# Optimization experiments

Hardware: AMD Instinct MI355X
Metric: run time of the kernel (lower is better)

The kernel has to match this reference:

```python
import jax, jax.numpy as jnp
import numpy as np

B, C, H, W = 8, 256, 64, 64
NH = 8
CM = 2048
EPS = 1e-5


def setup_inputs() -> dict:
    key = jax.random.key(0)
    ks = jax.random.split(key, 16)
    n = lambda k, s: (jax.random.normal(k, s, dtype=jnp.float32) * 0.02)
    return {
        'x': jax.random.normal(ks[0], (B, C, H, W), dtype=jnp.float32),
        'Wqkv': n(ks[1], (C, 3 * C)), 'bqkv': n(ks[2], (3 * C,)),
        'dw_w': n(ks[3], (C, 1, 3, 3)), 'dw_b': n(ks[4], (C,)),
        'Wproj': n(ks[5], (C, C)), 'bproj': n(ks[6], (C,)),
        'bn1_g': jnp.ones((C,), jnp.float32), 'bn1_b': jnp.zeros((C,), jnp.float32),
        'bn1_m': n(ks[7], (C,)), 'bn1_v': jax.random.uniform(ks[8], (C,), dtype=jnp.float32) + 0.5,
        'alpha1': jnp.ones((1,), jnp.float32),
        'Wfc1': n(ks[9], (C, CM)), 'bfc1': n(ks[10], (CM,)),
        'Wfc2': n(ks[11], (CM, C)), 'bfc2': n(ks[12], (C,)),
        'bn2_g': jnp.ones((C,), jnp.float32), 'bn2_b': jnp.zeros((C,), jnp.float32),
        'bn2_m': n(ks[13], (C,)), 'bn2_v': jax.random.uniform(ks[14], (C,), dtype=jnp.float32) + 0.5,
        'alpha2': jnp.ones((1,), jnp.float32),
    }


def _repbn(x, g, b, m, v, alpha):
    # eval-mode RepBN: BatchNorm1d with running stats over channel dim + alpha*x
    bn = (x - m) * jax.lax.rsqrt(v + EPS) * g + b
    return bn + alpha * x


def reference(x, Wqkv, bqkv, dw_w, dw_b, Wproj, bproj,
              bn1_g, bn1_b, bn1_m, bn1_v, alpha1,
              Wfc1, bfc1, Wfc2, bfc2,
              bn2_g, bn2_b, bn2_m, bn2_v, alpha2):
    b, c, h, w = x.shape
    n = h * w
    hd = c // NH
    scale = hd ** (-0.5)
    t = x.reshape(b, c, n).transpose(0, 2, 1)  # [B,N,C]

    # --- SimplifiedLinearAttention ---
    qkv = (t @ Wqkv + bqkv).reshape(b, n, 3, NH, hd).transpose(2, 0, 3, 1, 4)
    q, k, v = qkv[0], qkv[1], qkv[2]          # [B,H,N,hd]
    q = jax.nn.relu(q) * scale
    k = jax.nn.relu(k)
    ctx = jnp.einsum('bhnd,bhne->bhde', k, v)  # [B,H,hd,hd] small context
    out = jnp.einsum('bhnd,bhde->bhne', q, ctx)
    out = out.transpose(0, 2, 1, 3).reshape(b, n, c)
    img = out.transpose(0, 2, 1).reshape(b, c, h, w)
    img = jax.lax.conv_general_dilated(img, dw_w, (1, 1), 'SAME',
                                       feature_group_count=c)
    img = img + dw_b[None, :, None, None]
    out = img.reshape(b, c, n).transpose(0, 2, 1)
    out = out @ Wproj + bproj

    # residual + RepBN (eval branch of LinearNorm)
    t = _repbn(t + out, bn1_g, bn1_b, bn1_m, bn1_v, alpha1)

    # FFN (exact GELU as nn.GELU default)
    ff = jax.nn.gelu(t @ Wfc1 + bfc1, approximate=False) @ Wfc2 + bfc2
    t = _repbn(t + ff, bn2_g, bn2_b, bn2_m, bn2_v, alpha2)

    return t.transpose(0, 2, 1).reshape(b, c, h, w)
```

## Files before the change

### kernel.cpp

```cpp
#include <hip/hip_runtime.h>
#include <hip/hip_bf16.h>
#include <math.h>

constexpr int B_ = 8, C_ = 256, H_ = 64, W_ = 64;
constexpr int N_ = H_ * W_;
constexpr int NH_ = 8;
constexpr int CM_ = 2048;
constexpr int M_ = B_ * N_;
constexpr float EPS_ = 1e-5f;

typedef __bf16 bf16_t;
typedef bf16_t bf16x4 __attribute__((ext_vector_type(4)));
typedef bf16_t bf16x8 __attribute__((ext_vector_type(8)));
typedef float f32x4 __attribute__((ext_vector_type(4)));

__device__ inline bf16_t f2b(float f) {
    __hip_bfloat16 h = __float2bfloat16(f);
    return *reinterpret_cast<bf16_t*>(&h);
}
__device__ inline float b2f(bf16_t b) {
    unsigned short u = *reinterpret_cast<unsigned short*>(&b);
    unsigned int x = (unsigned int)u << 16;
    return *reinterpret_cast<float*>(&x);
}
__device__ inline unsigned pk2(float lo, float hi) {
    bf16_t l = f2b(lo), h = f2b(hi);
    unsigned short ls = *reinterpret_cast<unsigned short*>(&l);
    unsigned short hs = *reinterpret_cast<unsigned short*>(&h);
    return ((unsigned)hs << 16) | (unsigned)ls;
}
__device__ inline float gelu_ap(float y) {
    float u = y * (0.7978845608f + 0.0356774081f * y * y);
    float e = __expf(2.0f * u);
    return y - y * __builtin_amdgcn_rcpf(e + 1.0f);
}

#define GLOAD_LDS16(gptr, lptr)                                                     \
    __builtin_amdgcn_global_load_lds(                                               \
        (const __attribute__((address_space(1))) void*)(gptr),                      \
        (__attribute__((address_space(3))) void*)(lptr), 16, 0, 0)

__global__ __launch_bounds__(256)
void prep(const float* __restrict__ x, bf16_t* __restrict__ t_b,
          const float* __restrict__ Wqkv, bf16_t* __restrict__ WqkvT,
          const float* __restrict__ Wproj, bf16_t* __restrict__ WprojT,
          const float* __restrict__ Wfc1, bf16_t* __restrict__ Wfc1T,
          const float* __restrict__ Wfc2, bf16_t* __restrict__ Wfc2T) {
    __shared__ float tile[32][33];
    int id = blockIdx.x;
    int tx = threadIdx.x, ty = threadIdx.y;

    const float* src;
    bf16_t* dst;
    int K, N, k0, n0;

    if (id < 8192) {
        int b = id >> 10, rem = id & 1023;
        int nn = (rem & 127) * 32, cc = (rem >> 7) * 32;
#pragma unroll
        for (int i = ty; i < 32; i += 8)
            tile[i][tx] = x[(size_t)b * C_ * N_ + (size_t)(cc + i) * N_ + nn + tx];
        __syncthreads();
#pragma unroll
        for (int i = ty; i < 32; i += 8)
            t_b[(size_t)b * N_ * C_ + (size_t)(nn + i) * C_ + cc + tx] = f2b(tile[tx][i]);
        return;
    } else if (id < 8384) {
        int idw = id - 8192; K = C_; N = 768;
        n0 = (idw % 24) * 32; k0 = (idw / 24) * 32;
        src = Wqkv; dst = WqkvT;
    } else if (id < 8448) {
        int idw = id - 8384; K = C_; N = C_;
        n0 = (idw & 7) * 32; k0 = (idw >> 3) * 32;
        src = Wproj; dst = WprojT;
    } else if (id < 8960) {
        int idw = id - 8448; K = C_; N = CM_;
        n0 = (idw & 63) * 32; k0 = (idw >> 6) * 32;
        src = Wfc1; dst = Wfc1T;
    } else {
        int idw = id - 8960; K = CM_; N = C_;
        n0 = (idw & 7) * 32; k0 = (idw >> 3) * 32;
        src = Wfc2; dst = Wfc2T;
    }
#pragma unroll
    for (int i = ty; i < 32; i += 8)
        tile[i][tx] = src[(size_t)(k0 + i) * N + n0 + tx];
    __syncthreads();
#pragma unroll
    for (int i = ty; i < 32; i += 8)
        dst[(size_t)(n0 + i) * K + k0 + tx] = f2b(tile[tx][i]);
}

template <int EPI>
__global__ __launch_bounds__(256)
void gemm_swp(const bf16_t* __restrict__ Wt, const bf16_t* __restrict__ Act,
              const float* __restrict__ bias, bf16_t* __restrict__ Cb,
              int M, int N, int K,
              const bf16_t* __restrict__ tres_b,
              const float* __restrict__ g, const float* __restrict__ bb,
              const float* __restrict__ mm, const float* __restrict__ vv,
              const float* __restrict__ alpha) {
    __shared__ bf16x8 ldsv[4096];
    char* lds = (char*)ldsv;

    int tid  = threadIdx.x;
    int lane = tid & 63;
    int w    = tid >> 6;
    int wi   = w >> 1, wj = w & 1;

    int nwg = gridDim.x * gridDim.y;
    int bid = blockIdx.y * gridDim.x + blockIdx.x;
    int swz = (bid & 7) * (nwg >> 3) + (bid >> 3);
    int bx = swz % gridDim.x, by = swz / gridDim.x;
    int bch = bx * 128, bm = by * 128;

    int rowl = lane & 15, kq = lane >> 4;

#define STAGE_SWP(k0, p)                                                             \
    {                                                                                \
        _Pragma("unroll")                                                            \
        for (int j = 0; j < 4; ++j) {                                                \
            int jj = w * 4 + j;                                                      \
            int msub = jj >> 1, kh = jj & 1;                                         \
            const bf16_t* gw = Wt + ((size_t)(bch + msub * 16 + rowl) * K + (k0) +   \
                                     kh * 32 + kq * 8);                              \
            GLOAD_LDS16(gw, lds + (p) * 32768 + jj * 1024);                          \
            const bf16_t* ga = Act + ((size_t)(bm + msub * 16 + rowl) * K + (k0) +   \
                                      kh * 32 + kq * 8);                             \
            GLOAD_LDS16(ga, lds + (p) * 32768 + 16384 + jj * 1024);                  \
        }                                                                            \
    }

    f32x4 acc[4][4] = {};
    int T = K >> 6;

    STAGE_SWP(0, 0);
    __syncthreads();

    for (int t = 0; t < T; ++t) {
        int p = t & 1;
        if (t + 1 < T) STAGE_SWP((t + 1) << 6, p ^ 1);
#pragma unroll
        for (int ks = 0; ks < 2; ++ks) {
            bf16x8 wf[4], af[4];
#pragma unroll
            for (int i = 0; i < 4; ++i) wf[i] = ldsv[p * 2048 + ((wi * 4 + i) * 2 + ks) * 64 + lane];
#pragma unroll
            for (int j = 0; j < 4; ++j) af[j] = ldsv[p * 2048 + 1024 + ((wj * 4 + j) * 2 + ks) * 64 + lane];
#pragma unroll
            for (int i = 0; i < 4; ++i)
#pragma unroll
                for (int j = 0; j < 4; ++j)
                    acc[i][j] = __builtin_amdgcn_mfma_f32_16x16x32_bf16(wf[i], af[j], acc[i][j], 0, 0, 0);
        }
        if (t + 1 < T) __syncthreads();
    }

    float alpha_v = (EPI == 1) ? alpha[0] : 0.f;
#pragma unroll
    for (int i = 0; i < 4; ++i) {
        int ch = bch + wi * 64 + i * 16 + (lane >> 4) * 4;
        f32x4 b4 = *(const f32x4*)(bias + ch);
        f32x4 rs4, B4, m4;
        if (EPI == 1) {
            f32x4 g4 = *(const f32x4*)(g + ch);
            f32x4 v4 = *(const f32x4*)(vv + ch);
            B4 = *(const f32x4*)(bb + ch);
            m4 = *(const f32x4*)(mm + ch);
#pragma unroll
            for (int r = 0; r < 4; ++r) rs4[r] = rsqrtf(v4[r] + EPS_) * g4[r];
        }
#pragma unroll
        for (int j = 0; j < 4; ++j) {
            int m = bm + wj * 64 + j * 16 + (lane & 15);
            f32x4 a = acc[i][j];
            bf16_t ob[4];
            if (EPI == 4) {
#pragma unroll
                for (int r = 0; r < 4; ++r) ob[r] = f2b(a[r] + b4[r]);
            } else {
                bf16x4 t4 = *(const bf16x4*)(tres_b + (size_t)m * N + ch);
#pragma unroll
                for (int r = 0; r < 4; ++r) {
                    float z = b2f(t4[r]) + a[r] + b4[r];
                    ob[r] = f2b((z - m4[r]) * rs4[r] + B4[r] + alpha_v * z);
                }
            }
            *(bf16x4*)(Cb + (size_t)m * N + ch) = *(bf16x4*)ob;
        }
    }
}

__global__ __launch_bounds__(512, 2)
void ffn_fused(const bf16_t* __restrict__ Act, const bf16_t* __restrict__ W1t,
               const bf16_t* __restrict__ W2t,
               const float* __restrict__ bfc1, const float* __restrict__ bfc2,
               const float* __restrict__ g, const float* __restrict__ bb,
               const float* __restrict__ mm, const float* __restrict__ vv,
               const float* __restrict__ alpha, float* __restrict__ out) {
    __shared__ char lds[49152];
    bf16x8* ldsA = (bf16x8*)lds;
    bf16x8* ldsH = (bf16x8*)(lds + 32768);

    const int tid = threadIdx.x;
    const int lane = tid & 63;
    const int w = tid >> 6;
    const int l15 = lane & 15;
    const int kq = lane >> 4;
    const int m0 = blockIdx.x * 64;

#pragma unroll
    for (int j = 0; j < 4; ++j) {
        int jj = w * 4 + j;
        int mblk = jj >> 3, ks = jj & 7;
        const bf16_t* src = Act + (size_t)(m0 + mblk * 16 + l15) * 256 + ks * 32 + kq * 8;
        GLOAD_LDS16(src, lds + jj * 1024);
    }
    __syncthreads();

    f32x4 acc2[2][4] = {};

    const int hrow = w * 16 + l15;
    const int ks2w = w >> 1;
    const int lane2 = l15 + (((2 * w + (kq >> 1)) & 3) << 4);
    const int hwoff = (kq & 1) << 3;
    const int chb = w * 32;

    for (int c = 0; c < 16; ++c) {
        bf16x8 w1f[8];
#pragma unroll
        for (int ks = 0; ks < 8; ++ks)
            w1f[ks] = *(const bf16x8*)(W1t + (size_t)(c * 128 + hrow) * 256 + ks * 32 + kq * 8);
        f32x4 acc1[4] = {};
#pragma unroll
        for (int ks = 0; ks < 8; ++ks)
#pragma unroll
            for (int mblk = 0; mblk < 4; ++mblk)
                acc1[mblk] = __builtin_amdgcn_mfma_f32_16x16x32_bf16(
                    w1f[ks], ldsA[(mblk * 8 + ks) * 64 + lane], acc1[mblk], 0, 0, 0);

        f32x4 b1 = *(const f32x4*)(bfc1 + c * 128 + w * 16 + kq * 4);
#pragma unroll
        for (int mblk = 0; mblk < 4; ++mblk) {
            unsigned lo = pk2(gelu_ap(acc1[mblk][0] + b1[0]), gelu_ap(acc1[mblk][1] + b1[1]));
            unsigned hi = pk2(gelu_ap(acc1[mblk][2] + b1[2]), gelu_ap(acc1[mblk][3] + b1[3]));
            char* dst = lds + 32768 + (size_t)((mblk * 4 + ks2w) * 64 + lane2) * 16 + hwoff;
            *(unsigned*)dst = lo;
            *(unsigned*)(dst + 4) = hi;
        }
        __syncthreads();

        bf16x8 w2f[2][4];
#pragma unroll
        for (int cf = 0; cf < 2; ++cf)
#pragma unroll
            for (int ks2 = 0; ks2 < 4; ++ks2)
                w2f[cf][ks2] = *(const bf16x8*)(W2t + (size_t)(chb + cf * 16 + l15) * 2048 + c * 128 + ks2 * 32 + kq * 8);
#pragma unroll
        for (int mblk = 0; mblk < 4; ++mblk)
#pragma unroll
            for (int ks2 = 0; ks2 < 4; ++ks2) {
                bf16x8 hf = ldsH[(mblk * 4 + ks2) * 64 + lane];
                acc2[0][mblk] = __builtin_amdgcn_mfma_f32_16x16x32_bf16(hf, w2f[0][ks2], acc2[0][mblk], 0, 0, 0);
                acc2[1][mblk] = __builtin_amdgcn_mfma_f32_16x16x32_bf16(hf, w2f[1][ks2], acc2[1][mblk], 0, 0, 0);
            }
        __syncthreads();
    }

    float alpha_v = alpha[0];
#pragma unroll
    for (int cf = 0; cf < 2; ++cf) {
        int ch = chb + cf * 16 + l15;
        float b2v = bfc2[ch];
        float rs = rsqrtf(vv[ch] + EPS_) * g[ch];
        float bbv = bb[ch], mv = mm[ch];
#pragma unroll
        for (int mblk = 0; mblk < 4; ++mblk) {
            int mbase = m0 + mblk * 16 + kq * 4;
            f32x4 o4;
#pragma unroll
            for (int r = 0; r < 4; ++r) {
                float z = b2f(Act[(size_t)(mbase + r) * 256 + ch]) + acc2[cf][mblk][r] + b2v;
                o4[r] = (z - mv) * rs + bbv + alpha_v * z;
            }
            int bi = mbase >> 12, ni = mbase & (N_ - 1);
            *(f32x4*)(out + ((size_t)bi * C_ + ch) * N_ + ni) = o4;
        }
    }
}

__global__ void transpose_b(const bf16_t* __restrict__ in_, bf16_t* __restrict__ outb) {
    __shared__ float tile[32][33];
    int b  = blockIdx.z;
    int n0 = blockIdx.x * 32;
    int c0 = blockIdx.y * 32;
    int tx = threadIdx.x, ty = threadIdx.y;
#pragma unroll
    for (int i = ty; i < 32; i += 8)
        tile[i][tx] = b2f(in_[(size_t)b * C_ * N_ + (size_t)(c0 + i) * N_ + n0 + tx]);
    __syncthreads();
#pragma unroll
    for (int i = ty; i < 32; i += 8)
        outb[(size_t)b * N_ * C_ + (size_t)(n0 + i) * C_ + c0 + tx] = f2b(tile[tx][i]);
}

__global__ void ctx_partial(const bf16_t* __restrict__ qkv, float* __restrict__ ctxp) {
    __shared__ float kb[64][40];
    __shared__ float vb[64][40];
    int seg = blockIdx.x;
    int bh  = blockIdx.y;
    int b = bh >> 3, h = bh & 7;
    int tid = threadIdx.x;
    int d  = tid >> 3;
    int e0 = (tid & 7) * 4;
    int lrow = tid >> 2, lcol = (tid & 3) * 8;
    float acc[4] = {0.f, 0.f, 0.f, 0.f};
    const size_t base = (size_t)b * N_ * 768 + h * 32;
    for (int n0 = seg * 512; n0 < seg * 512 + 512; n0 += 64) {
        size_t ra = base + (size_t)(n0 + lrow) * 768 + lcol;
        bf16x8 kv8 = *(const bf16x8*)(qkv + ra + 256);
        bf16x8 vv8 = *(const bf16x8*)(qkv + ra + 512);
#pragma unroll
        for (int j = 0; j < 8; ++j) {
            kb[lrow][lcol + j] = b2f(kv8[j]);
            vb[lrow][lcol + j] = b2f(vv8[j]);
        }
        __syncthreads();
#pragma unroll
        for (int nl = 0; nl < 64; ++nl) {
            float kv = fmaxf(kb[nl][d], 0.f);
#pragma unroll
            for (int j = 0; j < 4; ++j)
                acc[j] = fmaf(kv, vb[nl][e0 + j], acc[j]);
        }
        __syncthreads();
    }
    float* o = ctxp + ((size_t)seg * 64 + bh) * 1024 + d * 32 + e0;
#pragma unroll
    for (int j = 0; j < 4; ++j) o[j] = acc[j];
}

__global__ void ctx_reduce(const float* __restrict__ ctxp, float* __restrict__ ctx) {
    int idx = blockIdx.x * 256 + threadIdx.x;
    float s = 0.f;
#pragma unroll
    for (int seg = 0; seg < 8; ++seg) s += ctxp[(size_t)seg * 65536 + idx];
    ctx[idx] = s;
}

__global__ void attn_out(const bf16_t* __restrict__ qkv, const float* __restrict__ ctx,
                         bf16_t* __restrict__ img) {
    __shared__ float qb[64][33];
    __shared__ float cs[32][32];
    int n0 = blockIdx.x * 64;
    int bh = blockIdx.y;
    int b = bh >> 3, h = bh & 7;
    int tid = threadIdx.x;
    const float scale = 0.17677669529663687f;
    {
        float4 vv = ((const float4*)(ctx + (size_t)bh * 1024))[tid];
        ((float4*)&cs[0][0])[tid] = vv;
    }
    const size_t base = (size_t)b * N_ * 768 + h * 32;
    int lrow = tid >> 2, lcol = (tid & 3) * 8;
    {
        bf16x8 q8 = *(const bf16x8*)(qkv + base + (size_t)(n0 + lrow) * 768 + lcol);
#pragma unroll
        for (int j = 0; j < 8; ++j)
            qb[lrow][lcol + j] = fmaxf(b2f(q8[j]), 0.f) * scale;
    }
    __syncthreads();
    int nl = tid & 63, ebase = tid >> 6;
    bf16_t* outp = img + ((size_t)b * C_ + h * 32) * N_ + n0 + nl;
#pragma unroll
    for (int p = 0; p < 8; ++p) {
        int e = ebase + p * 4;
        float s = 0.f;
#pragma unroll
        for (int dd = 0; dd < 32; ++dd)
            s = fmaf(qb[nl][dd], cs[dd][e], s);
        outp[(size_t)e * N_] = f2b(s);
    }
}

__global__ __launch_bounds__(256)
void dwconv3x3(const bf16_t* __restrict__ img, const float* __restrict__ w,
               const float* __restrict__ bias, bf16_t* __restrict__ out) {
    __shared__ float sp[64][65];
    int bc = blockIdx.x;
    int c  = bc & 255;
    int tid = threadIdx.x;
    const bf16_t* ip = img + (size_t)bc * N_;
#pragma unroll
    for (int l = 0; l < 2; ++l) {
        int flat = (tid + l * 256) * 8;
        int row = flat >> 6, col = flat & 63;
        bf16x8 v8 = *(const bf16x8*)(ip + flat);
#pragma unroll
        for (int j = 0; j < 8; ++j) sp[row][col + j] = b2f(v8[j]);
    }
    float wv[9];
#pragma unroll
    for (int j = 0; j < 9; ++j) wv[j] = w[c * 9 + j];
    float bv = bias[c];
    __syncthreads();

    int y = tid >> 2, x0 = (tid & 3) * 16;
    float o[16];
#pragma unroll
    for (int i = 0; i < 16; ++i) o[i] = bv;
#pragma unroll
    for (int dy = -1; dy <= 1; ++dy) {
        int yy = y + dy;
        if (yy < 0 || yy > 63) continue;
#pragma unroll
        for (int dx = -1; dx <= 1; ++dx) {
            float wgt = wv[(dy + 1) * 3 + dx + 1];
#pragma unroll
            for (int i = 0; i < 16; ++i) {
                int xx = x0 + i + dx;
                float val = (xx < 0 || xx > 63) ? 0.f : sp[yy][xx];
                o[i] = fmaf(wgt, val, o[i]);
            }
        }
    }
    bf16_t ob[16];
#pragma unroll
    for (int i = 0; i < 16; ++i) ob[i] = f2b(o[i]);
    *(bf16x8*)(out + (size_t)bc * N_ + y * 64 + x0)     = *(bf16x8*)&ob[0];
    *(bf16x8*)(out + (size_t)bc * N_ + y * 64 + x0 + 8) = *(bf16x8*)&ob[8];
}

extern "C" void kernel_launch(void* const* d_in, const int* in_sizes, int n_in,
                              void* d_out, int out_size, void* d_ws, size_t ws_size,
                              hipStream_t stream) {
    const float* x     = (const float*)d_in[0];
    const float* Wqkv  = (const float*)d_in[1];
    const float* bqkv  = (const float*)d_in[2];
    const float* dw_w  = (const float*)d_in[3];
    const float* dw_b  = (const float*)d_in[4];
    const float* Wproj = (const float*)d_in[5];
    const float* bproj = (const float*)d_in[6];
    const float* bn1_g = (const float*)d_in[7];
    const float* bn1_b = (const float*)d_in[8];
    const float* bn1_m = (const float*)d_in[9];
    const float* bn1_v = (const float*)d_in[10];
    const float* alpha1= (const float*)d_in[11];
    const float* Wfc1  = (const float*)d_in[12];
    const float* bfc1  = (const float*)d_in[13];
    const float* Wfc2  = (const float*)d_in[14];
    const float* bfc2  = (const float*)d_in[15];
    const float* bn2_g = (const float*)d_in[16];
    const float* bn2_b = (const float*)d_in[17];
    const float* bn2_m = (const float*)d_in[18];
    const float* bn2_v = (const float*)d_in[19];
    const float* alpha2= (const float*)d_in[20];
    float* out = (float*)d_out;

    char* ws = (char*)d_ws;
    bf16_t* t_b2    = (bf16_t*)(ws);
    bf16_t* WqkvT   = (bf16_t*)(ws + 16777216);
    bf16_t* WprojT  = (bf16_t*)(ws + 17170432);
    bf16_t* Wfc1T   = (bf16_t*)(ws + 17301504);
    bf16_t* Wfc2T   = (bf16_t*)(ws + 18350080);
    float*  ctxp    = (float*)(ws + 19398656);
    float*  ctx     = (float*)(ws + 21495808);
    bf16_t* t_b     = (bf16_t*)(ws + 21757952);
    bf16_t* qkv_b   = (bf16_t*)(ws + 38535168);
    bf16_t* img_b   = (bf16_t*)(ws + 88866816);
    bf16_t* conv_b  = (bf16_t*)(ws + 105644032);
    bf16_t* convT_b = (bf16_t*)(ws + 122421248);

    prep<<<9472, dim3(32, 8), 0, stream>>>(x, t_b, Wqkv, WqkvT, Wproj, WprojT,
                                           Wfc1, Wfc1T, Wfc2, Wfc2T);

    gemm_swp<4><<<dim3(768 / 128, M_ / 128), 256, 0, stream>>>(
        WqkvT, t_b, bqkv, qkv_b, M_, 768, C_,
        nullptr, nullptr, nullptr, nullptr, nullptr, nullptr);

    ctx_partial<<<dim3(8, B_ * NH_), 256, 0, stream>>>(qkv_b, ctxp);
    ctx_reduce<<<256, 256, 0, stream>>>(ctxp, ctx);

    attn_out<<<dim3(N_ / 64, B_ * NH_), 256, 0, stream>>>(qkv_b, ctx, img_b);

    dwconv3x3<<<B_ * C_, 256, 0, stream>>>(img_b, dw_w, dw_b, conv_b);

    transpose_b<<<dim3(N_ / 32, C_ / 32, B_), dim3(32, 8), 0, stream>>>(conv_b, convT_b);

    gemm_swp<1><<<dim3(C_ / 128, M_ / 128), 256, 0, stream>>>(
        WprojT, convT_b, bproj, t_b2, M_, C_, C_,
        t_b, bn1_g, bn1_b, bn1_m, bn1_v, alpha1);

    ffn_fused<<<M_ / 64, 512, 0, stream>>>(
        t_b2, Wfc1T, Wfc2T, bfc1, bfc2,
        bn2_g, bn2_b, bn2_m, bn2_v, alpha2, out);
}
```

Before: 303.7 us.

## Trade GEMM LDS double-buffering for occupancy; prefetch W1 and double-buffer H in FFN

The generic GEMM drops its double-buffered LDS staging in favour of a single buffer with two barriers per K step, halving LDS use, and raises launch bounds to 4 blocks per CU. In the fused FFN, the next chunk's W1 fragments are prefetched into registers and the GELU hidden tile is double-buffered in LDS, which removes one barrier per chunk. The cost is less load/compute overlap in the GEMM, and possible spills or limited occupancy in the FFN under the tighter register budget, while its LDS grows to 64KB.

```diff
diff --git a/kernel.cpp b/kernel.cpp
--- a/kernel.cpp
+++ b/kernel.cpp
@@ -92,7 +92,7 @@
 }
 
 template <int EPI>
-__global__ __launch_bounds__(256)
+__global__ __launch_bounds__(256, 4)
 void gemm_swp(const bf16_t* __restrict__ Wt, const bf16_t* __restrict__ Act,
               const float* __restrict__ bias, bf16_t* __restrict__ Cb,
               int M, int N, int K,
@@ -100,7 +100,7 @@
               const float* __restrict__ g, const float* __restrict__ bb,
               const float* __restrict__ mm, const float* __restrict__ vv,
               const float* __restrict__ alpha) {
-    __shared__ bf16x8 ldsv[4096];
+    __shared__ bf16x8 ldsv[2048];
     char* lds = (char*)ldsv;
 
     int tid  = threadIdx.x;
@@ -116,44 +116,33 @@
 
     int rowl = lane & 15, kq = lane >> 4;
 
-#define STAGE_SWP(k0, p)                                                             \
-    {                                                                                \
-        _Pragma("unroll")                                                            \
-        for (int j = 0; j < 4; ++j) {                                                \
-            int jj = w * 4 + j;                                                      \
-            int msub = jj >> 1, kh = jj & 1;                                         \
-            const bf16_t* gw = Wt + ((size_t)(bch + msub * 16 + rowl) * K + (k0) +   \
-                                     kh * 32 + kq * 8);                              \
-            GLOAD_LDS16(gw, lds + (p) * 32768 + jj * 1024);                          \
-            const bf16_t* ga = Act + ((size_t)(bm + msub * 16 + rowl) * K + (k0) +   \
-                                      kh * 32 + kq * 8);                             \
-            GLOAD_LDS16(ga, lds + (p) * 32768 + 16384 + jj * 1024);                  \
-        }                                                                            \
-    }
-
     f32x4 acc[4][4] = {};
-    int T = K >> 6;
-
-    STAGE_SWP(0, 0);
-    __syncthreads();
-
-    for (int t = 0; t < T; ++t) {
-        int p = t & 1;
-        if (t + 1 < T) STAGE_SWP((t + 1) << 6, p ^ 1);
+
+    for (int k0 = 0; k0 < K; k0 += 64) {
+#pragma unroll
+        for (int j = 0; j < 4; ++j) {
+            int jj = w * 4 + j;
+            int msub = jj >> 1, kh = jj & 1;
+            const bf16_t* gw = Wt + ((size_t)(bch + msub * 16 + rowl) * K + k0 + kh * 32 + kq * 8);
+            GLOAD_LDS16(gw, lds + jj * 1024);
+            const bf16_t* ga = Act + ((size_t)(bm + msub * 16 + rowl) * K + k0 + kh * 32 + kq * 8);
+            GLOAD_LDS16(ga, lds + 16384 + jj * 1024);
+        }
+        __syncthreads();
 #pragma unroll
         for (int ks = 0; ks < 2; ++ks) {
             bf16x8 wf[4], af[4];
 #pragma unroll
-            for (int i = 0; i < 4; ++i) wf[i] = ldsv[p * 2048 + ((wi * 4 + i) * 2 + ks) * 64 + lane];
-#pragma unroll
-            for (int j = 0; j < 4; ++j) af[j] = ldsv[p * 2048 + 1024 + ((wj * 4 + j) * 2 + ks) * 64 + lane];
+            for (int i = 0; i < 4; ++i) wf[i] = ldsv[((wi * 4 + i) * 2 + ks) * 64 + lane];
+#pragma unroll
+            for (int j = 0; j < 4; ++j) af[j] = ldsv[1024 + ((wj * 4 + j) * 2 + ks) * 64 + lane];
 #pragma unroll
             for (int i = 0; i < 4; ++i)
 #pragma unroll
                 for (int j = 0; j < 4; ++j)
                     acc[i][j] = __builtin_amdgcn_mfma_f32_16x16x32_bf16(wf[i], af[j], acc[i][j], 0, 0, 0);
         }
-        if (t + 1 < T) __syncthreads();
+        __syncthreads();
     }
 
     float alpha_v = (EPI == 1) ? alpha[0] : 0.f;
@@ -191,16 +180,15 @@
     }
 }
 
-__global__ __launch_bounds__(512, 2)
+__global__ __launch_bounds__(512, 4)
 void ffn_fused(const bf16_t* __restrict__ Act, const bf16_t* __restrict__ W1t,
                const bf16_t* __restrict__ W2t,
                const float* __restrict__ bfc1, const float* __restrict__ bfc2,
                const float* __restrict__ g, const float* __restrict__ bb,
                const float* __restrict__ mm, const float* __restrict__ vv,
                const float* __restrict__ alpha, float* __restrict__ out) {
-    __shared__ char lds[49152];
+    __shared__ char lds[65536];
     bf16x8* ldsA = (bf16x8*)lds;
-    bf16x8* ldsH = (bf16x8*)(lds + 32768);
 
     const int tid = threadIdx.x;
     const int lane = tid & 63;
@@ -226,11 +214,12 @@
     const int hwoff = (kq & 1) << 3;
     const int chb = w * 32;
 
+    bf16x8 w1f[8];
+#pragma unroll
+    for (int ks = 0; ks < 8; ++ks)
+        w1f[ks] = *(const bf16x8*)(W1t + (size_t)hrow * 256 + ks * 32 + kq * 8);
+
     for (int c = 0; c < 16; ++c) {
-        bf16x8 w1f[8];
-#pragma unroll
-        for (int ks = 0; ks < 8; ++ks)
-            w1f[ks] = *(const bf16x8*)(W1t + (size_t)(c * 128 + hrow) * 256 + ks * 32 + kq * 8);
         f32x4 acc1[4] = {};
 #pragma unroll
         for (int ks = 0; ks < 8; ++ks)
@@ -239,23 +228,30 @@
                 acc1[mblk] = __builtin_amdgcn_mfma_f32_16x16x32_bf16(
                     w1f[ks], ldsA[(mblk * 8 + ks) * 64 + lane], acc1[mblk], 0, 0, 0);
 
-        f32x4 b1 = *(const f32x4*)(bfc1 + c * 128 + w * 16 + kq * 4);
-#pragma unroll
-        for (int mblk = 0; mblk < 4; ++mblk) {
-            unsigned lo = pk2(gelu_ap(acc1[mblk][0] + b1[0]), gelu_ap(acc1[mblk][1] + b1[1]));
-            unsigned hi = pk2(gelu_ap(acc1[mblk][2] + b1[2]), gelu_ap(acc1[mblk][3] + b1[3]));
-            char* dst = lds + 32768 + (size_t)((mblk * 4 + ks2w) * 64 + lane2) * 16 + hwoff;
-            *(unsigned*)dst = lo;
-            *(unsigned*)(dst + 4) = hi;
-        }
-        __syncthreads();
-
+        if (c + 1 < 16) {
+#pragma unroll
+            for (int ks = 0; ks < 8; ++ks)
+                w1f[ks] = *(const bf16x8*)(W1t + (size_t)((c + 1) * 128 + hrow) * 256 + ks * 32 + kq * 8);
+        }
         bf16x8 w2f[2][4];
 #pragma unroll
         for (int cf = 0; cf < 2; ++cf)
 #pragma unroll
             for (int ks2 = 0; ks2 < 4; ++ks2)
                 w2f[cf][ks2] = *(const bf16x8*)(W2t + (size_t)(chb + cf * 16 + l15) * 2048 + c * 128 + ks2 * 32 + kq * 8);
+
+        f32x4 b1 = *(const f32x4*)(bfc1 + c * 128 + w * 16 + kq * 4);
+        char* hbase = lds + 32768 + (c & 1) * 16384;
+#pragma unroll
+        for (int mblk = 0; mblk < 4; ++mblk) {
+            uint2 u2;
+            u2.x = pk2(gelu_ap(acc1[mblk][0] + b1[0]), gelu_ap(acc1[mblk][1] + b1[1]));
+            u2.y = pk2(gelu_ap(acc1[mblk][2] + b1[2]), gelu_ap(acc1[mblk][3] + b1[3]));
+            *(uint2*)(hbase + (size_t)((mblk * 4 + ks2w) * 64 + lane2) * 16 + hwoff) = u2;
+        }
+        __syncthreads();
+
+        bf16x8* ldsH = (bf16x8*)(lds + 32768 + (c & 1) * 16384);
 #pragma unroll
         for (int mblk = 0; mblk < 4; ++mblk)
 #pragma unroll
@@ -264,7 +260,6 @@
                 acc2[0][mblk] = __builtin_amdgcn_mfma_f32_16x16x32_bf16(hf, w2f[0][ks2], acc2[0][mblk], 0, 0, 0);
                 acc2[1][mblk] = __builtin_amdgcn_mfma_f32_16x16x32_bf16(hf, w2f[1][ks2], acc2[1][mblk], 0, 0, 0);
             }
-        __syncthreads();
     }
 
     float alpha_v = alpha[0];
```

New measurement: 296.6 us. 2.3% less time.
